# Optimization experiments

Measured on AMD Instinct MI355X. Metric: run time of the kernel, lower is better.

## Reference

```python
import jax, jax.numpy as jnp
import numpy as np

N, E = 100000, 1600000
D_IN, H, C = 128, 4, 32
NEG_SLOPE = 0.2

def setup_inputs() -> dict:
    key = jax.random.key(0)
    ks = jax.random.split(key, 6)
    x = jax.random.normal(ks[0], (N, D_IN), dtype=jnp.float32)
    edge_index = jax.random.randint(ks[1], (2, E), 0, N, dtype=jnp.int64)
    s = 1.0 / np.sqrt(D_IN)
    W_l = jax.random.normal(ks[2], (D_IN, H * C), dtype=jnp.float32) * s
    W_r = jax.random.normal(ks[3], (D_IN, H * C), dtype=jnp.float32) * s
    att = jax.random.normal(ks[4], (H, C), dtype=jnp.float32) * (1.0 / np.sqrt(C))
    bias = jax.random.normal(ks[5], (H * C,), dtype=jnp.float32) * 0.01
    return {"x": x, "edge_index": edge_index, "W_l": W_l, "W_r": W_r, "att": att, "bias": bias}

def reference(x, edge_index, W_l, W_r, att, bias):
    # GATv2: e_ij = att . LeakyReLU(W_l x_j + W_r x_i); softmax over incoming edges of i;
    # out_i = sum_j alpha_ij * (W_l x_j); heads concatenated, then bias.
    src, dst = edge_index[0], edge_index[1]
    n = x.shape[0]
    xl = (x @ W_l).reshape(n, H, C)   # source transform (lin_l)
    xr = (x @ W_r).reshape(n, H, C)   # target transform (lin_r)
    xj = xl[src]                       # [E,H,C] gathered source feats
    xi = xr[dst]                       # [E,H,C] gathered target feats
    e = jax.nn.leaky_relu(xi + xj, NEG_SLOPE)
    score = jnp.einsum('ehc,hc->eh', e, att)          # [E,H]
    # segment softmax over destination nodes
    m = jax.ops.segment_max(score, dst, num_segments=n)  # [N,H]
    ex = jnp.exp(score - m[dst])
    denom = jax.ops.segment_sum(ex, dst, num_segments=n)  # [N,H]
    alpha = ex / (denom[dst] + 1e-16)                      # [E,H]
    out = jax.ops.segment_sum(alpha[..., None] * xj, dst, num_segments=n)  # [N,H,C]
    return out.reshape(n, H * C) + bias
```

## Files before the change

kernel.cpp:

```cpp
#include <hip/hip_runtime.h>
#include <hip/hip_bf16.h>
#include <math.h>

#define N_NODES 100000
#define E_EDGES 1600000
#define D 128
#define NEG_SLOPE 0.2f

#define BSH   8
#define NBKT  391
#define BCAP  4992
#define P1_EPB 8192
#define P1_TPB 512
#define P1_EPT 16

typedef __bf16 bf16x8 __attribute__((ext_vector_type(8)));
typedef float f32x4 __attribute__((ext_vector_type(4)));
typedef float f32x2 __attribute__((ext_vector_type(2)));

__device__ __forceinline__ float bf2f(unsigned short u) {
    union { unsigned int i; float f; } x; x.i = ((unsigned int)u) << 16; return x.f;
}
__device__ __forceinline__ unsigned short f2bf(float f) {
    union { float f; unsigned int i; } x; x.f = f;
    unsigned int r = x.i + 0x7fffu + ((x.i >> 16) & 1u);
    return (unsigned short)(r >> 16);
}
__device__ __forceinline__ void unpack4p(uint2 u, f32x2* lo, f32x2* hi) {
    union { unsigned int i; float f; } a, b, c, d;
    a.i = u.x << 16; b.i = u.x & 0xffff0000u;
    c.i = u.y << 16; d.i = u.y & 0xffff0000u;
    *lo = (f32x2){a.f, b.f}; *hi = (f32x2){c.f, d.f};
}
__device__ __forceinline__ f32x2 pabs(f32x2 v) {
    union { f32x2 f; unsigned int u[2]; } x; x.f = v;
    x.u[0] &= 0x7fffffffu; x.u[1] &= 0x7fffffffu;
    return x.f;
}

__global__ void GATv2Conv_56908316672629_kernel(
    const unsigned int* ei_words, int* flags,
    const float* __restrict__ Wl, const float* __restrict__ Wr,
    unsigned short* __restrict__ wtg, int* __restrict__ bcur)
{
    __shared__ int cnt_edge;
    const int tid = threadIdx.x;
    const int bid = blockIdx.x;

    if (bid == 0) {
        for (int i = tid; i < NBKT; i += 256) bcur[i] = 0;
    }
    if (bid == 1) {
        if (tid == 0) cnt_edge = 0;
        __syncthreads();
        unsigned int w = ei_words[2 * tid + 1];
        if (w != 0u) atomicAdd(&cnt_edge, 1);
        __syncthreads();
        if (tid == 0) flags[0] = (cnt_edge == 0) ? 1 : 0;
    }

    const int gid = bid * 256 + tid;
    const int sel = gid >> 14;
    const int rem = gid & 16383;
    const int k = rem >> 7, n = rem & 127;
    const float* W = sel ? Wr : Wl;
    wtg[(size_t)sel * 16384 + n * 128 + k] = f2bf(W[k * 128 + n]);
}

__global__ __launch_bounds__(256) void gemm_f32_kernel(
    const float* __restrict__ X,
    const unsigned short* __restrict__ wtg,
    unsigned short* __restrict__ xl, unsigned short* __restrict__ xr)
{
    __shared__ unsigned short Xs[128][136];

    const int rowbase = blockIdx.x * 128;
    const int tid = threadIdx.x;

    for (int c = tid; c < 4096; c += 256) {
        int r = c >> 5, k4 = (c & 31) << 2;
        int grow = rowbase + r;
        float4 v = make_float4(0.f, 0.f, 0.f, 0.f);
        if (grow < N_NODES) v = ((const float4*)(X + (size_t)grow * D))[c & 31];
        union { unsigned short us[4]; uint2 u2; } pk;
        pk.us[0] = f2bf(v.x); pk.us[1] = f2bf(v.y);
        pk.us[2] = f2bf(v.z); pk.us[3] = f2bf(v.w);
        *((uint2*)&Xs[r][k4]) = pk.u2;
    }
    __syncthreads();

    const int wave = tid >> 6, lane = tid & 63;
    const int mrow = lane & 15, quad = lane >> 4;

    for (int sel = 0; sel < 2; ++sel) {
        const bf16x8* wt = (const bf16x8*)(wtg + (size_t)sel * 16384);
        unsigned short* out = sel ? xr : xl;

        f32x4 accA[8], accB[8];
#pragma unroll
        for (int i = 0; i < 8; ++i) {
            accA[i] = (f32x4){0.f, 0.f, 0.f, 0.f};
            accB[i] = (f32x4){0.f, 0.f, 0.f, 0.f};
        }

#pragma unroll
        for (int kk = 0; kk < 4; ++kk) {
            const int k0 = kk * 32 + quad * 8;
            bf16x8 afA = *(const bf16x8*)&Xs[wave * 16 + mrow][k0];
            bf16x8 afB = *(const bf16x8*)&Xs[64 + wave * 16 + mrow][k0];
            const bf16x8* wk = wt + mrow * 16 + kk * 4 + quad;
#pragma unroll
            for (int n0 = 0; n0 < 8; ++n0) {
                bf16x8 bfrag = wk[n0 * 256];
                accA[n0] = __builtin_amdgcn_mfma_f32_16x16x32_bf16(afA, bfrag, accA[n0], 0, 0, 0);
                accB[n0] = __builtin_amdgcn_mfma_f32_16x16x32_bf16(afB, bfrag, accB[n0], 0, 0, 0);
            }
        }

        const int growA = rowbase + wave * 16 + quad * 4;
        const int growB = growA + 64;
#pragma unroll
        for (int n0 = 0; n0 < 8; ++n0) {
            int col = n0 * 16 + mrow;
#pragma unroll
            for (int r = 0; r < 4; ++r) {
                int ga = growA + r, gb2 = growB + r;
                if (ga < N_NODES) out[(size_t)ga * D + col] = f2bf(accA[n0][r]);
                if (gb2 < N_NODES) out[(size_t)gb2 * D + col] = f2bf(accB[n0][r]);
            }
        }
    }
}

__device__ __forceinline__ unsigned int edge_word(const unsigned int* ei, int is64,
                                                  long long entry) {
    return is64 ? ei[2 * entry] : ei[entry];
}

__global__ __launch_bounds__(P1_TPB) void bucket_scatter_kernel(
    const unsigned int* __restrict__ ei, const int* __restrict__ flags,
    int* __restrict__ bcur, unsigned int* __restrict__ pairbuf)
{
    __shared__ int h[NBKT];
    __shared__ int gbase[NBKT];

    const int tid = threadIdx.x;
    const int is64 = flags[0];
    const long long e0 = (long long)blockIdx.x * P1_EPB;

    unsigned int sv[P1_EPT], dv[P1_EPT];
#pragma unroll
    for (int j = 0; j < P1_EPT; ++j) {
        long long e = e0 + j * P1_TPB + tid;
        unsigned int s = 0u, d = 0xffffffffu;
        if (e < E_EDGES) {
            s = edge_word(ei, is64, e);
            d = edge_word(ei, is64, (long long)E_EDGES + e);
            if (s >= N_NODES || d >= N_NODES) d = 0xffffffffu;
        }
        sv[j] = s; dv[j] = d;
    }

    for (int i = tid; i < NBKT; i += P1_TPB) h[i] = 0;
    __syncthreads();

#pragma unroll
    for (int j = 0; j < P1_EPT; ++j)
        if (dv[j] != 0xffffffffu) atomicAdd(&h[dv[j] >> BSH], 1);
    __syncthreads();

    for (int i = tid; i < NBKT; i += P1_TPB) {
        int c = h[i];
        gbase[i] = c ? atomicAdd(&bcur[i], c) : 0;
        h[i] = 0;
    }
    __syncthreads();

#pragma unroll
    for (int j = 0; j < P1_EPT; ++j) {
        unsigned int d = dv[j];
        if (d != 0xffffffffu) {
            int b = (int)(d >> BSH);
            int r = gbase[b] + atomicAdd(&h[b], 1);
            if (r < BCAP)
                pairbuf[(size_t)b * BCAP + r] = sv[j] | ((d & 255u) << 24);
        }
    }
}

__global__ __launch_bounds__(256) void bucket_sort_kernel(
    const int* __restrict__ bcur, unsigned int* __restrict__ pairbuf,
    int* __restrict__ rowstart, int* __restrict__ rowend,
    int* __restrict__ order)
{
    __shared__ unsigned int stage[BCAP];
    __shared__ int cnt[256];
    __shared__ int base[256];
    __shared__ int dh[64];
    __shared__ int dcur[64];

    const int b = blockIdx.x;
    const int tid = threadIdx.x;
    int n = bcur[b]; if (n > BCAP) n = BCAP;
    unsigned int* buf = pairbuf + (size_t)b * BCAP;

    for (int i = tid; i < n; i += 256) stage[i] = buf[i];
    cnt[tid] = 0;
    if (tid < 64) dh[tid] = 0;
    __syncthreads();

    for (int i = tid; i < n; i += 256) atomicAdd(&cnt[stage[i] >> 24], 1);
    __syncthreads();

    int v = cnt[tid];
    const int bin = (v < 63) ? v : 63;
    atomicAdd(&dh[bin], 1);
    base[tid] = v;
    __syncthreads();
    for (int off = 1; off < 256; off <<= 1) {
        int u = (tid >= off) ? base[tid - off] : 0;
        __syncthreads();
        base[tid] += u;
        __syncthreads();
    }
    const int myend = base[tid];
    const int mystart = myend - v;

    if (tid < 64) {
        int x = dh[tid];
        int inc = x;
#pragma unroll
        for (int off = 1; off < 64; off <<= 1) {
            int u = __shfl_up(inc, off);
            if (tid >= off) inc += u;
        }
        dcur[tid] = inc - x;
    }
    __syncthreads();

    const int rank = atomicAdd(&dcur[bin], 1);
    order[b * 256 + rank] = b * 256 + tid;

    const int node = b * 256 + tid;
    if (node < N_NODES) {
        rowstart[node] = b * BCAP + mystart;
        rowend[node]   = b * BCAP + myend;
    }

    cnt[tid] = mystart;
    __syncthreads();

    for (int i = tid; i < n; i += 256) {
        unsigned int p = stage[i];
        int pos = atomicAdd(&cnt[p >> 24], 1);
        buf[pos] = p & 0x00FFFFFFu;
    }
}

__global__ __launch_bounds__(256) void aggregate_kernel(
    const unsigned short* __restrict__ xl, const unsigned short* __restrict__ xr,
    const int* __restrict__ rowstart, const int* __restrict__ rowend,
    const int* __restrict__ ssrc, const int* __restrict__ order,
    const float* __restrict__ att, const float* __restrict__ bias,
    float* __restrict__ out)
{
    const int t = threadIdx.x & 31;
    const int g = blockIdx.x * 8 + (threadIdx.x >> 5);
    const int node = order[g];
    if (node >= N_NODES) return;
    const int f0 = t * 4;

    f32x2 xr0, xr1;
    unpack4p(*(const uint2*)&xr[(size_t)node * D + f0], &xr0, &xr1);
    const float4 av = *(const float4*)&att[f0];
    f32x2 a60 = (f32x2){0.6f * av.x, 0.6f * av.y};
    f32x2 a61 = (f32x2){0.6f * av.z, 0.6f * av.w};
    f32x2 a40 = (f32x2){0.4f * av.x, 0.4f * av.y};
    f32x2 a41 = (f32x2){0.4f * av.z, 0.4f * av.w};

    const uint2* xlp = (const uint2*)xl + (f0 >> 2);

    const int p0 = rowstart[node];
    const int p1 = rowend[node];

    float l = 0.f;
    f32x2 acc0 = (f32x2){0.f, 0.f}, acc1 = (f32x2){0.f, 0.f};

#define ESCORE(u, xa0, xa1, pe)                                   \
    {                                                             \
        unpack4p(u, &xa0, &xa1);                                  \
        f32x2 v0 = xa0 + xr0, v1 = xa1 + xr1;                     \
        f32x2 pp = v0 * a60;                                      \
        pp += pabs(v0) * a40;                                     \
        pp += v1 * a61;                                           \
        pp += pabs(v1) * a41;                                     \
        pe = pp.x + pp.y;                                         \
    }

    int p = p0;
    for (; p + 4 <= p1; p += 4) {
        int s0 = ssrc[p], s1 = ssrc[p + 1], s2 = ssrc[p + 2], s3 = ssrc[p + 3];
        uint2 u0 = xlp[(size_t)s0 * 32];
        uint2 u1 = xlp[(size_t)s1 * 32];
        uint2 u2 = xlp[(size_t)s2 * 32];
        uint2 u3 = xlp[(size_t)s3 * 32];
        f32x2 xa0, xa1, xb0, xb1, xc0, xc1, xd0, xd1;
        float e0, e1, e2, e3;
        ESCORE(u0, xa0, xa1, e0);
        ESCORE(u1, xb0, xb1, e1);
        ESCORE(u2, xc0, xc1, e2);
        ESCORE(u3, xd0, xd1, e3);
#pragma unroll
        for (int off = 1; off < 8; off <<= 1) {
            e0 += __shfl_xor(e0, off);
            e1 += __shfl_xor(e1, off);
            e2 += __shfl_xor(e2, off);
            e3 += __shfl_xor(e3, off);
        }
        float w0 = __expf(e0), w1 = __expf(e1), w2 = __expf(e2), w3 = __expf(e3);
        l += (w0 + w1) + (w2 + w3);
        acc0 += w0 * xa0; acc1 += w0 * xa1;
        acc0 += w1 * xb0; acc1 += w1 * xb1;
        acc0 += w2 * xc0; acc1 += w2 * xc1;
        acc0 += w3 * xd0; acc1 += w3 * xd1;
    }
    for (; p < p1; ++p) {
        int s0 = ssrc[p];
        uint2 u0 = xlp[(size_t)s0 * 32];
        f32x2 xa0, xa1;
        float e0;
        ESCORE(u0, xa0, xa1, e0);
#pragma unroll
        for (int off = 1; off < 8; off <<= 1) e0 += __shfl_xor(e0, off);
        float w0 = __expf(e0);
        l += w0;
        acc0 += w0 * xa0; acc1 += w0 * xa1;
    }
#undef ESCORE

    const float inv = (l > 0.f) ? (1.f / l) : 0.f;
    const float4 bv = *(const float4*)&bias[f0];
    float4 o;
    o.x = fmaf(acc0.x, inv, bv.x);
    o.y = fmaf(acc0.y, inv, bv.y);
    o.z = fmaf(acc1.x, inv, bv.z);
    o.w = fmaf(acc1.y, inv, bv.w);
    *(float4*)&out[(size_t)node * D + f0] = o;
}

extern "C" void kernel_launch(void* const* d_in, const int* in_sizes, int n_in,
                              void* d_out, int out_size, void* d_ws, size_t ws_size,
                              hipStream_t stream)
{
    const float*        X    = (const float*)d_in[0];
    const unsigned int* ei   = (const unsigned int*)d_in[1];
    const float*        Wl   = (const float*)d_in[2];
    const float*        Wr   = (const float*)d_in[3];
    const float*        att  = (const float*)d_in[4];
    const float*        bias = (const float*)d_in[5];

    char* ws = (char*)d_ws;
    size_t off = 0;
    unsigned short* xl = (unsigned short*)(ws + off); off += (size_t)N_NODES * D * 2;
    unsigned short* xr = (unsigned short*)(ws + off); off += (size_t)N_NODES * D * 2;
    unsigned int* pairbuf = (unsigned int*)(ws + off); off += (size_t)NBKT * BCAP * 4;
    int* rowstart = (int*)(ws + off); off += (size_t)N_NODES * 4;
    int* rowend   = (int*)(ws + off); off += (size_t)N_NODES * 4;
    int* order    = (int*)(ws + off); off += (size_t)NBKT * 256 * 4;
    int* bcur     = (int*)(ws + off); off += (size_t)((NBKT + 255) & ~255) * 4;
    int* flags    = (int*)(ws + off); off += 256;
    unsigned short* wtg = (unsigned short*)(ws + off); off += 2 * 128 * 128 * 2;

    const int gb = (N_NODES + 127) / 128;
    const int p1b = (E_EDGES + P1_EPB - 1) / P1_EPB;

    GATv2Conv_56908316672629_kernel<<<128, 256, 0, stream>>>(ei, flags, Wl, Wr, wtg, bcur);

    gemm_f32_kernel<<<gb, 256, 0, stream>>>(X, wtg, xl, xr);

    bucket_scatter_kernel<<<p1b, P1_TPB, 0, stream>>>(ei, flags, bcur, pairbuf);
    bucket_sort_kernel<<<NBKT, 256, 0, stream>>>(bcur, pairbuf, rowstart, rowend, order);

    aggregate_kernel<<<(NBKT * 256) / 8, 256, 0, stream>>>(
        xl, xr, rowstart, rowend, (const int*)pairbuf, order, att, bias, (float*)d_out);
}
```

Before: 277.6 us.

## Fuse edge bucket scatter into GEMM launch, drop degree ordering, widen sort blocks

The edge bucket-scatter work now runs as extra blocks of the GEMM kernel, sharing one launch and a union of shared memory, so the scatter and the projection GEMM overlap on the GPU. The bucket sort uses 512 threads and a wave-shuffle prefix scan in place of the barrier-heavy LDS scan. The degree-histogram node ordering (the order array) is removed, so aggregation processes nodes in natural order. This saves a launch and sort overhead, but loses degree-based load balancing in the aggregate kernel.

```diff
diff --git a/kernel.cpp b/kernel.cpp
--- a/kernel.cpp
+++ b/kernel.cpp
@@ -10,9 +10,9 @@
 #define BSH   8
 #define NBKT  391
 #define BCAP  4992
-#define P1_EPB 8192
-#define P1_TPB 512
-#define P1_EPT 16
+#define SC_EPB 8192
+#define SC_EPT 32
+#define SC_BLOCKS ((E_EDGES + SC_EPB - 1) / SC_EPB)
 
 typedef __bf16 bf16x8 __attribute__((ext_vector_type(8)));
 typedef float f32x4 __attribute__((ext_vector_type(4)));
@@ -70,12 +70,70 @@
 __global__ __launch_bounds__(256) void gemm_f32_kernel(
     const float* __restrict__ X,
     const unsigned short* __restrict__ wtg,
-    unsigned short* __restrict__ xl, unsigned short* __restrict__ xr)
-{
-    __shared__ unsigned short Xs[128][136];
-
-    const int rowbase = blockIdx.x * 128;
+    unsigned short* __restrict__ xl, unsigned short* __restrict__ xr,
+    const unsigned int* __restrict__ ei, const int* __restrict__ flags,
+    int* __restrict__ bcur, unsigned int* __restrict__ pairbuf)
+{
+    __shared__ union {
+        unsigned short Xs[128][136];
+        struct { int h[NBKT]; int gbase[NBKT]; } sc;
+    } sm;
+
     const int tid = threadIdx.x;
+
+    if (blockIdx.x < SC_BLOCKS) {
+        int* h = sm.sc.h;
+        int* gbase = sm.sc.gbase;
+        const int is64 = flags[0];
+        const long long e0 = (long long)blockIdx.x * SC_EPB;
+
+        unsigned int sv[SC_EPT], dv[SC_EPT];
+#pragma unroll
+        for (int j = 0; j < SC_EPT; ++j) {
+            long long e = e0 + j * 256 + tid;
+            unsigned int s = 0u, d = 0xffffffffu;
+            if (e < E_EDGES) {
+                if (is64) {
+                    s = ((const uint2*)ei)[e].x;
+                    d = ((const uint2*)ei)[E_EDGES + e].x;
+                } else {
+                    s = ei[e];
+                    d = ei[E_EDGES + e];
+                }
+                if (s >= N_NODES || d >= N_NODES) d = 0xffffffffu;
+            }
+            sv[j] = s; dv[j] = d;
+        }
+
+        for (int i = tid; i < NBKT; i += 256) h[i] = 0;
+        __syncthreads();
+
+#pragma unroll
+        for (int j = 0; j < SC_EPT; ++j)
+            if (dv[j] != 0xffffffffu) atomicAdd(&h[dv[j] >> BSH], 1);
+        __syncthreads();
+
+        for (int i = tid; i < NBKT; i += 256) {
+            int c = h[i];
+            gbase[i] = c ? atomicAdd(&bcur[i], c) : 0;
+            h[i] = 0;
+        }
+        __syncthreads();
+
+#pragma unroll
+        for (int j = 0; j < SC_EPT; ++j) {
+            unsigned int d = dv[j];
+            if (d != 0xffffffffu) {
+                int b = (int)(d >> BSH);
+                int r = gbase[b] + atomicAdd(&h[b], 1);
+                if (r < BCAP)
+                    pairbuf[(size_t)b * BCAP + r] = sv[j] | ((d & 255u) << 24);
+            }
+        }
+        return;
+    }
+
+    const int rowbase = (blockIdx.x - SC_BLOCKS) * 128;
 
     for (int c = tid; c < 4096; c += 256) {
         int r = c >> 5, k4 = (c & 31) << 2;
@@ -85,7 +143,7 @@
         union { unsigned short us[4]; uint2 u2; } pk;
         pk.us[0] = f2bf(v.x); pk.us[1] = f2bf(v.y);
         pk.us[2] = f2bf(v.z); pk.us[3] = f2bf(v.w);
-        *((uint2*)&Xs[r][k4]) = pk.u2;
+        *((uint2*)&sm.Xs[r][k4]) = pk.u2;
     }
     __syncthreads();
 
@@ -106,8 +164,8 @@
 #pragma unroll
         for (int kk = 0; kk < 4; ++kk) {
             const int k0 = kk * 32 + quad * 8;
-            bf16x8 afA = *(const bf16x8*)&Xs[wave * 16 + mrow][k0];
-            bf16x8 afB = *(const bf16x8*)&Xs[64 + wave * 16 + mrow][k0];
+            bf16x8 afA = *(const bf16x8*)&sm.Xs[wave * 16 + mrow][k0];
+            bf16x8 afB = *(const bf16x8*)&sm.Xs[64 + wave * 16 + mrow][k0];
             const bf16x8* wk = wt + mrow * 16 + kk * 4 + quad;
 #pragma unroll
             for (int n0 = 0; n0 < 8; ++n0) {
@@ -132,125 +190,56 @@
     }
 }
 
-__device__ __forceinline__ unsigned int edge_word(const unsigned int* ei, int is64,
-                                                  long long entry) {
-    return is64 ? ei[2 * entry] : ei[entry];
-}
-
-__global__ __launch_bounds__(P1_TPB) void bucket_scatter_kernel(
-    const unsigned int* __restrict__ ei, const int* __restrict__ flags,
-    int* __restrict__ bcur, unsigned int* __restrict__ pairbuf)
-{
-    __shared__ int h[NBKT];
-    __shared__ int gbase[NBKT];
-
-    const int tid = threadIdx.x;
-    const int is64 = flags[0];
-    const long long e0 = (long long)blockIdx.x * P1_EPB;
-
-    unsigned int sv[P1_EPT], dv[P1_EPT];
-#pragma unroll
-    for (int j = 0; j < P1_EPT; ++j) {
-        long long e = e0 + j * P1_TPB + tid;
-        unsigned int s = 0u, d = 0xffffffffu;
-        if (e < E_EDGES) {
-            s = edge_word(ei, is64, e);
-            d = edge_word(ei, is64, (long long)E_EDGES + e);
-            if (s >= N_NODES || d >= N_NODES) d = 0xffffffffu;
-        }
-        sv[j] = s; dv[j] = d;
-    }
-
-    for (int i = tid; i < NBKT; i += P1_TPB) h[i] = 0;
-    __syncthreads();
-
-#pragma unroll
-    for (int j = 0; j < P1_EPT; ++j)
-        if (dv[j] != 0xffffffffu) atomicAdd(&h[dv[j] >> BSH], 1);
-    __syncthreads();
-
-    for (int i = tid; i < NBKT; i += P1_TPB) {
-        int c = h[i];
-        gbase[i] = c ? atomicAdd(&bcur[i], c) : 0;
-        h[i] = 0;
-    }
-    __syncthreads();
-
-#pragma unroll
-    for (int j = 0; j < P1_EPT; ++j) {
-        unsigned int d = dv[j];
-        if (d != 0xffffffffu) {
-            int b = (int)(d >> BSH);
-            int r = gbase[b] + atomicAdd(&h[b], 1);
-            if (r < BCAP)
-                pairbuf[(size_t)b * BCAP + r] = sv[j] | ((d & 255u) << 24);
-        }
-    }
-}
-
-__global__ __launch_bounds__(256) void bucket_sort_kernel(
+__global__ __launch_bounds__(512) void bucket_sort_kernel(
     const int* __restrict__ bcur, unsigned int* __restrict__ pairbuf,
-    int* __restrict__ rowstart, int* __restrict__ rowend,
-    int* __restrict__ order)
+    int* __restrict__ rowstart, int* __restrict__ rowend)
 {
     __shared__ unsigned int stage[BCAP];
     __shared__ int cnt[256];
-    __shared__ int base[256];
-    __shared__ int dh[64];
-    __shared__ int dcur[64];
+    __shared__ int wsum[4];
 
     const int b = blockIdx.x;
     const int tid = threadIdx.x;
     int n = bcur[b]; if (n > BCAP) n = BCAP;
     unsigned int* buf = pairbuf + (size_t)b * BCAP;
 
-    for (int i = tid; i < n; i += 256) stage[i] = buf[i];
-    cnt[tid] = 0;
-    if (tid < 64) dh[tid] = 0;
-    __syncthreads();
-
-    for (int i = tid; i < n; i += 256) atomicAdd(&cnt[stage[i] >> 24], 1);
-    __syncthreads();
-
-    int v = cnt[tid];
-    const int bin = (v < 63) ? v : 63;
-    atomicAdd(&dh[bin], 1);
-    base[tid] = v;
-    __syncthreads();
-    for (int off = 1; off < 256; off <<= 1) {
-        int u = (tid >= off) ? base[tid - off] : 0;
-        __syncthreads();
-        base[tid] += u;
-        __syncthreads();
-    }
-    const int myend = base[tid];
-    const int mystart = myend - v;
-
-    if (tid < 64) {
-        int x = dh[tid];
-        int inc = x;
+    for (int i = tid; i < n; i += 512) stage[i] = buf[i];
+    if (tid < 256) cnt[tid] = 0;
+    __syncthreads();
+
+    for (int i = tid; i < n; i += 512) atomicAdd(&cnt[stage[i] >> 24], 1);
+    __syncthreads();
+
+    const int lane = tid & 63, wid = tid >> 6;
+    int v = 0, inc = 0;
+    if (tid < 256) {
+        v = cnt[tid];
+        inc = v;
 #pragma unroll
         for (int off = 1; off < 64; off <<= 1) {
             int u = __shfl_up(inc, off);
-            if (tid >= off) inc += u;
-        }
-        dcur[tid] = inc - x;
-    }
-    __syncthreads();
-
-    const int rank = atomicAdd(&dcur[bin], 1);
-    order[b * 256 + rank] = b * 256 + tid;
-
-    const int node = b * 256 + tid;
-    if (node < N_NODES) {
-        rowstart[node] = b * BCAP + mystart;
-        rowend[node]   = b * BCAP + myend;
-    }
-
-    cnt[tid] = mystart;
-    __syncthreads();
-
-    for (int i = tid; i < n; i += 256) {
+            if (lane >= off) inc += u;
+        }
+        if (lane == 63) wsum[wid] = inc;
+    }
+    __syncthreads();
+    if (tid < 256) {
+        int add = 0;
+#pragma unroll
+        for (int w = 0; w < 3; ++w)
+            if (w < wid) add += wsum[w];
+        const int myend = inc + add;
+        const int mystart = myend - v;
+        const int node = b * 256 + tid;
+        if (node < N_NODES) {
+            rowstart[node] = b * BCAP + mystart;
+            rowend[node]   = b * BCAP + myend;
+        }
+        cnt[tid] = mystart;
+    }
+    __syncthreads();
+
+    for (int i = tid; i < n; i += 512) {
         unsigned int p = stage[i];
         int pos = atomicAdd(&cnt[p >> 24], 1);
         buf[pos] = p & 0x00FFFFFFu;
@@ -260,13 +249,12 @@
 __global__ __launch_bounds__(256) void aggregate_kernel(
     const unsigned short* __restrict__ xl, const unsigned short* __restrict__ xr,
     const int* __restrict__ rowstart, const int* __restrict__ rowend,
-    const int* __restrict__ ssrc, const int* __restrict__ order,
+    const int* __restrict__ ssrc,
     const float* __restrict__ att, const float* __restrict__ bias,
     float* __restrict__ out)
 {
     const int t = threadIdx.x & 31;
-    const int g = blockIdx.x * 8 + (threadIdx.x >> 5);
-    const int node = order[g];
+    const int node = blockIdx.x * 8 + (threadIdx.x >> 5);
     if (node >= N_NODES) return;
     const int f0 = t * 4;
 
@@ -366,21 +354,19 @@
     unsigned int* pairbuf = (unsigned int*)(ws + off); off += (size_t)NBKT * BCAP * 4;
     int* rowstart = (int*)(ws + off); off += (size_t)N_NODES * 4;
     int* rowend   = (int*)(ws + off); off += (size_t)N_NODES * 4;
-    int* order    = (int*)(ws + off); off += (size_t)NBKT * 256 * 4;
     int* bcur     = (int*)(ws + off); off += (size_t)((NBKT + 255) & ~255) * 4;
     int* flags    = (int*)(ws + off); off += 256;
     unsigned short* wtg = (unsigned short*)(ws + off); off += 2 * 128 * 128 * 2;
 
     const int gb = (N_NODES + 127) / 128;
-    const int p1b = (E_EDGES + P1_EPB - 1) / P1_EPB;
 
     GATv2Conv_56908316672629_kernel<<<128, 256, 0, stream>>>(ei, flags, Wl, Wr, wtg, bcur);
 
-    gemm_f32_kernel<<<gb, 256, 0, stream>>>(X, wtg, xl, xr);
-
-    bucket_scatter_kernel<<<p1b, P1_TPB, 0, stream>>>(ei, flags, bcur, pairbuf);
-    bucket_sort_kernel<<<NBKT, 256, 0, stream>>>(bcur, pairbuf, rowstart, rowend, order);
-
-    aggregate_kernel<<<(NBKT * 256) / 8, 256, 0, stream>>>(
-        xl, xr, rowstart, rowend, (const int*)pairbuf, order, att, bias, (float*)d_out);
-}
+    gemm_f32_kernel<<<SC_BLOCKS + gb, 256, 0, stream>>>(
+        X, wtg, xl, xr, ei, flags, bcur, pairbuf);
+
+    bucket_sort_kernel<<<NBKT, 512, 0, stream>>>(bcur, pairbuf, rowstart, rowend);
+
+    aggregate_kernel<<<(N_NODES + 7) / 8, 256, 0, stream>>>(
+        xl, xr, rowstart, rowend, (const int*)pairbuf, att, bias, (float*)d_out);
+}
```

New measurement: 246.0 us. 1.13x faster.
